# Performance work log

Hardware: AMD Instinct MI355X
Metric: run time of the kernel (lower is better)

The kernel has to match this reference:

```python
import jax, jax.numpy as jnp
import numpy as np
from jax import lax

B, L, H, K = 256, 512, 768, 64


def setup_inputs() -> dict:
    key = jax.random.key(0)
    k1, k2, k3, k4, k5 = jax.random.split(key, 5)
    features = jax.random.normal(k1, (B, L, H), dtype=jnp.float32)
    W = jax.random.normal(k2, (H, K), dtype=jnp.float32) * 0.02
    b = jnp.zeros((K,), dtype=jnp.float32)
    transition = jax.random.normal(k3, (K, K), dtype=jnp.float32)
    tags = jax.random.randint(k4, (B, L), 0, K, dtype=jnp.int64)
    # variable sentence lengths in decreasing order (repo sorts batches by length)
    lengths = jnp.sort(jax.random.randint(k5, (B,), L // 4, L + 1))[::-1]
    mask = jnp.arange(L)[None, :] < lengths[:, None]  # (B, L) bool, pads at end
    return {"features": features, "W": W, "b": b, "transition": transition,
            "tags": tags, "mask": mask}


def reference(features, W, b, transition, tags, mask):
    # encode: hidden2tag linear (dropout is identity in eval)
    emit = jnp.einsum("blh,hk->blk", features, W) + b  # (B, L, K)
    maskf = mask.astype(emit.dtype)

    # gold path score
    gold_emit = jnp.take_along_axis(emit, tags[:, :, None], axis=2)[..., 0]  # (B, L)
    trans_sc = transition[tags[:, :-1], tags[:, 1:]]                          # (B, L-1)
    score = gold_emit.at[:, 1:].add(trans_sc)
    total_score = (score * maskf).sum(axis=1)                                 # (B,)

    # CRF forward algorithm (log partition) via scan over time
    d0 = emit[:, 0]  # (B, K)
    emit_t = jnp.moveaxis(emit[:, 1:], 1, 0)  # (L-1, B, K)
    mask_t = mask[:, 1:].T                    # (L-1, B)

    def step(d, xs):
        e_t, m_t = xs
        # log_sum[b, j, k] = d[b, j] + transition[j, k] + e_t[b, k]
        log_sum = d[:, :, None] + transition[None, :, :] + e_t[:, None, :]
        d_new = jax.scipy.special.logsumexp(log_sum, axis=1)  # (B, K)
        d = jnp.where(m_t[:, None], d_new, d)  # finished sequences keep old d
        return d, None

    d, _ = lax.scan(step, d0, (emit_t, mask_t))
    log_z = jax.scipy.special.logsumexp(d, axis=1)  # (B,)

    return log_z - total_score  # negative log-likelihood per sentence, (B,)
```

## Files before the change

kernel.cpp:

```cpp
#include <hip/hip_runtime.h>
#include <hip/hip_bf16.h>
#include <string.h>

#define B_ 256
#define L_ 512
#define H_ 768
#define K_ 64
#define WT_OFF 33554432

typedef float  float4v  __attribute__((ext_vector_type(4)));
typedef float  float2v  __attribute__((ext_vector_type(2)));
typedef short  short8v  __attribute__((ext_vector_type(8)));

union BFragU { uint4 u4; short8v s8; };

__device__ inline unsigned short f2bf_bits(float f) {
    union { float f; unsigned int u; } c; c.f = f;
    unsigned int u = c.u;
    u += 0x7fffu + ((u >> 16) & 1u);
    return (unsigned short)(u >> 16);
}

__device__ inline float2v mk2(float x, float y) { float2v v; v.x = x; v.y = y; return v; }

__global__ void wt_transpose(const float* __restrict__ W, unsigned int* __restrict__ Wt) {
    int k = blockIdx.x;
    int j = threadIdx.x;
    float a = W[(size_t)(2 * j) * K_ + k];
    float b = W[(size_t)(2 * j + 1) * K_ + k];
    unsigned int u = (unsigned int)f2bf_bits(a) | ((unsigned int)f2bf_bits(b) << 16);
    Wt[k * (H_ / 2) + j] = u;
}

__global__ __launch_bounds__(256, 4)
void emit_gemm(const float* __restrict__ A, const unsigned short* __restrict__ Wt,
               const float* __restrict__ bias, float* __restrict__ emit) {
    const int tid  = threadIdx.x;
    const int lane = tid & 63;
    const int wid  = tid >> 6;
    const int lm   = lane & 15;
    const int lq   = lane >> 4;

    float4v acc[2][4];
    #pragma unroll
    for (int c = 0; c < 2; ++c)
        #pragma unroll
        for (int nt = 0; nt < 4; ++nt)
            acc[c][nt] = (float4v)0.f;

    const int rowbase = blockIdx.x * 128 + wid * 16 + lm;

    for (int ks = 0; ks < 24; ++ks) {
        short8v bfrag[4];
        #pragma unroll
        for (int nt = 0; nt < 4; ++nt) {
            const uint4* bp = reinterpret_cast<const uint4*>(
                Wt + (size_t)(lm + nt * 16) * H_ + ks * 32 + lq * 8);
            BFragU bb; bb.u4 = *bp;
            bfrag[nt] = bb.s8;
        }
        #pragma unroll
        for (int c = 0; c < 2; ++c) {
            const float* ap = A + (size_t)(rowbase + c * 64) * H_ + ks * 32 + lq * 8;
            float4 a0 = *reinterpret_cast<const float4*>(ap);
            float4 a1 = *reinterpret_cast<const float4*>(ap + 4);
            __hip_bfloat162 tt[4];
            tt[0] = __float22bfloat162_rn(make_float2(a0.x, a0.y));
            tt[1] = __float22bfloat162_rn(make_float2(a0.z, a0.w));
            tt[2] = __float22bfloat162_rn(make_float2(a1.x, a1.y));
            tt[3] = __float22bfloat162_rn(make_float2(a1.z, a1.w));
            short8v afrag;
            memcpy(&afrag, tt, 16);
            #pragma unroll
            for (int nt = 0; nt < 4; ++nt)
                acc[c][nt] = __builtin_amdgcn_mfma_f32_16x16x32_bf16(
                    afrag, bfrag[nt], acc[c][nt], 0, 0, 0);
        }
    }

    float bv[4];
    #pragma unroll
    for (int nt = 0; nt < 4; ++nt) bv[nt] = bias[nt * 16 + lm];
    #pragma unroll
    for (int c = 0; c < 2; ++c) {
        int rowb = blockIdx.x * 128 + c * 64 + wid * 16 + lq * 4;
        #pragma unroll
        for (int nt = 0; nt < 4; ++nt) {
            int col = nt * 16 + lm;
            #pragma unroll
            for (int r = 0; r < 4; ++r)
                emit[(size_t)(rowb + r) * K_ + col] = acc[c][nt][r] + bv[nt];
        }
    }
}

__global__ __launch_bounds__(64, 1)
void crf_scan(const float* __restrict__ emit, const float* __restrict__ T,
              const int* __restrict__ tags, const int* __restrict__ mask,
              float* __restrict__ out) {
    const int b    = blockIdx.x;
    const int lane = threadIdx.x;
    __shared__ __align__(16) float ebuf[2][16 * 64];
    __shared__ __align__(16) float qbuf[2][64];

    int len = 0;
    #pragma unroll
    for (int j = 0; j < 8; ++j) len += (mask[b * L_ + j * 64 + lane] != 0);
    #pragma unroll
    for (int off = 32; off; off >>= 1) len += __shfl_xor(len, off, 64);

    float2v et2[32];
    #pragma unroll
    for (int j = 0; j < 32; ++j) {
        et2[j].x = __expf(T[(2 * j) * K_ + lane]);
        et2[j].y = __expf(T[(2 * j + 1) * K_ + lane]);
    }

    const float* eb = emit + (size_t)b * L_ * K_;

    float sc = 0.f;
    for (int t = lane; t < len; t += 64) {
        int tg = tags[b * L_ + t];
        sc += eb[(size_t)t * K_ + tg];
        if (t > 0) sc += T[tags[b * L_ + t - 1] * K_ + tg];
    }
    #pragma unroll
    for (int off = 32; off; off >>= 1) sc += __shfl_xor(sc, off, 64);

    float e00 = eb[lane];
    float M = __int_as_float(__builtin_amdgcn_readfirstlane(__float_as_int(e00)));
    float q = __expf(e00 - M);
    qbuf[0][lane] = q;
    int prev_eps = 0;

    const int soff = ((lane >> 2) << 6) + ((lane & 3) << 4);
    {
        const float4* src = reinterpret_cast<const float4*>(eb + soff);
        float4 r0 = src[0], r1 = src[1], r2 = src[2], r3 = src[3];
        float4* dst = reinterpret_cast<float4*>(&ebuf[0][soff]);
        dst[0] = r0; dst[1] = r1; dst[2] = r2; dst[3] = r3;
    }

    int cur = 0;
    int t = 1;
    for (int c = 0;; ++c) {
        const int nt0  = (c + 1) << 4;
        const bool more = nt0 < len;
        float4 r0, r1, r2, r3;
        if (more) {
            const float4* src = reinterpret_cast<const float4*>(eb + nt0 * K_ + soff);
            r0 = src[0]; r1 = src[1]; r2 = src[2]; r3 = src[3];
        }
        const int tend = more ? nt0 : len;
        for (; t < tend; ++t) {
            float e  = ebuf[cur][((t & 15) << 6) + lane];
            float ef = __int_as_float(__builtin_amdgcn_readfirstlane(__float_as_int(e)));
            float delta = (float)prev_eps * 0.69314718f + ef;
            M += delta;
            float f = __expf(e - delta);

            const float4* qb4 = reinterpret_cast<const float4*>(&qbuf[(t + 1) & 1][0]);
            float2v a0 = mk2(0.f, 0.f), a1 = mk2(0.f, 0.f);
            float2v a2 = mk2(0.f, 0.f), a3 = mk2(0.f, 0.f);
            #pragma unroll
            for (int r = 0; r < 16; r += 2) {
                float4 p0 = qb4[r];
                float4 p1 = qb4[r + 1];
                a0 += mk2(p0.x, p0.y) * et2[2 * r];
                a1 += mk2(p0.z, p0.w) * et2[2 * r + 1];
                a2 += mk2(p1.x, p1.y) * et2[2 * r + 2];
                a3 += mk2(p1.z, p1.w) * et2[2 * r + 3];
            }
            float2v s2 = (a0 + a1) + (a2 + a3);
            float s = s2.x + s2.y;
            unsigned su = (unsigned)__builtin_amdgcn_readfirstlane(__float_as_int(s));
            prev_eps = (int)((su >> 23) & 0xff) - 127;
            q = s * f;
            qbuf[t & 1][lane] = q;
        }
        if (!more) break;
        float4* dst = reinterpret_cast<float4*>(&ebuf[cur ^ 1][soff]);
        dst[0] = r0; dst[1] = r1; dst[2] = r2; dst[3] = r3;
        cur ^= 1;
    }

    float z = q;
    #pragma unroll
    for (int off = 32; off; off >>= 1) z += __shfl_xor(z, off, 64);
    if (lane == 0) out[b] = M + __logf(z) - sc;
}

extern "C" void kernel_launch(void* const* d_in, const int* in_sizes, int n_in,
                              void* d_out, int out_size, void* d_ws, size_t ws_size,
                              hipStream_t stream) {
    const float* feat = (const float*)d_in[0];
    const float* W    = (const float*)d_in[1];
    const float* bias = (const float*)d_in[2];
    const float* T    = (const float*)d_in[3];
    const int*   tags = (const int*)d_in[4];
    const int*   mask = (const int*)d_in[5];
    float* out  = (float*)d_out;
    float* emit = (float*)d_ws;
    unsigned int*   WtW = (unsigned int*)((char*)d_ws + WT_OFF);
    unsigned short* Wt  = (unsigned short*)WtW;

    hipLaunchKernelGGL(wt_transpose, dim3(K_),   dim3(H_ / 2), 0, stream, W, WtW);
    hipLaunchKernelGGL(emit_gemm,    dim3(1024), dim3(256),    0, stream, feat, Wt, bias, emit);
    hipLaunchKernelGGL(crf_scan,     dim3(B_),   dim3(64),     0, stream, emit, T, tags, mask, out);
}
```

Baseline: 745.6 us.

## Skip padded rows in emission GEMM and double-buffer its global loads

The emission GEMM now reads the mask and exits blocks whose first row is padding. When only the second 64-row half of a block is padding, it runs a one-chunk variant that skips that half. Padded emissions are never read by the scan, so this avoids loading feature data that does not affect the output. The K loop is also software-pipelined with two register stages so loads overlap the MFMA work. In exchange, register pressure rises and occupancy is lowered to 2 blocks per CU.

```diff
diff --git a/kernel.cpp b/kernel.cpp
--- a/kernel.cpp
+++ b/kernel.cpp
@@ -32,58 +32,81 @@
     Wt[k * (H_ / 2) + j] = u;
 }
 
-__global__ __launch_bounds__(256, 4)
-void emit_gemm(const float* __restrict__ A, const unsigned short* __restrict__ Wt,
-               const float* __restrict__ bias, float* __restrict__ emit) {
-    const int tid  = threadIdx.x;
+template<int NC>
+struct Stage {
+    uint4  b[4];
+    float4 a[NC][2];
+};
+
+template<int NC>
+__device__ __forceinline__ void load_stage(Stage<NC>& s, const float* __restrict__ A,
+        const unsigned short* __restrict__ Wt, int rowbase, int ks, int lm, int lq) {
+    #pragma unroll
+    for (int nt = 0; nt < 4; ++nt)
+        s.b[nt] = *reinterpret_cast<const uint4*>(
+            Wt + (size_t)(lm + nt * 16) * H_ + ks * 32 + lq * 8);
+    #pragma unroll
+    for (int c = 0; c < NC; ++c) {
+        const float* ap = A + (size_t)(rowbase + c * 64) * H_ + ks * 32 + lq * 8;
+        s.a[c][0] = *reinterpret_cast<const float4*>(ap);
+        s.a[c][1] = *reinterpret_cast<const float4*>(ap + 4);
+    }
+}
+
+template<int NC>
+__device__ __forceinline__ void consume_stage(const Stage<NC>& s, float4v acc[][4]) {
+    short8v bfrag[4];
+    #pragma unroll
+    for (int nt = 0; nt < 4; ++nt) { BFragU u; u.u4 = s.b[nt]; bfrag[nt] = u.s8; }
+    #pragma unroll
+    for (int c = 0; c < NC; ++c) {
+        __hip_bfloat162 tt[4];
+        tt[0] = __float22bfloat162_rn(make_float2(s.a[c][0].x, s.a[c][0].y));
+        tt[1] = __float22bfloat162_rn(make_float2(s.a[c][0].z, s.a[c][0].w));
+        tt[2] = __float22bfloat162_rn(make_float2(s.a[c][1].x, s.a[c][1].y));
+        tt[3] = __float22bfloat162_rn(make_float2(s.a[c][1].z, s.a[c][1].w));
+        short8v afrag;
+        memcpy(&afrag, tt, 16);
+        #pragma unroll
+        for (int nt = 0; nt < 4; ++nt)
+            acc[c][nt] = __builtin_amdgcn_mfma_f32_16x16x32_bf16(
+                afrag, bfrag[nt], acc[c][nt], 0, 0, 0);
+    }
+}
+
+template<int NC>
+__device__ __forceinline__ void gemm_body(const float* __restrict__ A,
+        const unsigned short* __restrict__ Wt, const float* __restrict__ bias,
+        float* __restrict__ emit, int blk, int tid) {
     const int lane = tid & 63;
     const int wid  = tid >> 6;
     const int lm   = lane & 15;
     const int lq   = lane >> 4;
-
-    float4v acc[2][4];
-    #pragma unroll
-    for (int c = 0; c < 2; ++c)
+    const int rowbase = blk * 128 + wid * 16 + lm;
+
+    float4v acc[NC][4];
+    #pragma unroll
+    for (int c = 0; c < NC; ++c)
         #pragma unroll
         for (int nt = 0; nt < 4; ++nt)
             acc[c][nt] = (float4v)0.f;
 
-    const int rowbase = blockIdx.x * 128 + wid * 16 + lm;
-
-    for (int ks = 0; ks < 24; ++ks) {
-        short8v bfrag[4];
-        #pragma unroll
-        for (int nt = 0; nt < 4; ++nt) {
-            const uint4* bp = reinterpret_cast<const uint4*>(
-                Wt + (size_t)(lm + nt * 16) * H_ + ks * 32 + lq * 8);
-            BFragU bb; bb.u4 = *bp;
-            bfrag[nt] = bb.s8;
-        }
-        #pragma unroll
-        for (int c = 0; c < 2; ++c) {
-            const float* ap = A + (size_t)(rowbase + c * 64) * H_ + ks * 32 + lq * 8;
-            float4 a0 = *reinterpret_cast<const float4*>(ap);
-            float4 a1 = *reinterpret_cast<const float4*>(ap + 4);
-            __hip_bfloat162 tt[4];
-            tt[0] = __float22bfloat162_rn(make_float2(a0.x, a0.y));
-            tt[1] = __float22bfloat162_rn(make_float2(a0.z, a0.w));
-            tt[2] = __float22bfloat162_rn(make_float2(a1.x, a1.y));
-            tt[3] = __float22bfloat162_rn(make_float2(a1.z, a1.w));
-            short8v afrag;
-            memcpy(&afrag, tt, 16);
-            #pragma unroll
-            for (int nt = 0; nt < 4; ++nt)
-                acc[c][nt] = __builtin_amdgcn_mfma_f32_16x16x32_bf16(
-                    afrag, bfrag[nt], acc[c][nt], 0, 0, 0);
-        }
+    Stage<NC> s0, s1;
+    load_stage<NC>(s0, A, Wt, rowbase, 0, lm, lq);
+    #pragma unroll 1
+    for (int ks = 0; ks < 24; ks += 2) {
+        load_stage<NC>(s1, A, Wt, rowbase, ks + 1, lm, lq);
+        consume_stage<NC>(s0, acc);
+        load_stage<NC>(s0, A, Wt, rowbase, (ks + 2 < 24) ? ks + 2 : 23, lm, lq);
+        consume_stage<NC>(s1, acc);
     }
 
     float bv[4];
     #pragma unroll
     for (int nt = 0; nt < 4; ++nt) bv[nt] = bias[nt * 16 + lm];
     #pragma unroll
-    for (int c = 0; c < 2; ++c) {
-        int rowb = blockIdx.x * 128 + c * 64 + wid * 16 + lq * 4;
+    for (int c = 0; c < NC; ++c) {
+        int rowb = blk * 128 + c * 64 + wid * 16 + lq * 4;
         #pragma unroll
         for (int nt = 0; nt < 4; ++nt) {
             int col = nt * 16 + lm;
@@ -92,6 +115,18 @@
                 emit[(size_t)(rowb + r) * K_ + col] = acc[c][nt][r] + bv[nt];
         }
     }
+}
+
+__global__ __launch_bounds__(256, 2)
+void emit_gemm(const float* __restrict__ A, const unsigned short* __restrict__ Wt,
+               const float* __restrict__ bias, const int* __restrict__ mask,
+               float* __restrict__ emit) {
+    const int r0 = blockIdx.x * 128;
+    if (mask[r0] == 0) return;
+    if (mask[r0 + 64])
+        gemm_body<2>(A, Wt, bias, emit, blockIdx.x, threadIdx.x);
+    else
+        gemm_body<1>(A, Wt, bias, emit, blockIdx.x, threadIdx.x);
 }
 
 __global__ __launch_bounds__(64, 1)
@@ -205,6 +240,6 @@
     unsigned short* Wt  = (unsigned short*)WtW;
 
     hipLaunchKernelGGL(wt_transpose, dim3(K_),   dim3(H_ / 2), 0, stream, W, WtW);
-    hipLaunchKernelGGL(emit_gemm,    dim3(1024), dim3(256),    0, stream, feat, Wt, bias, emit);
+    hipLaunchKernelGGL(emit_gemm,    dim3(1024), dim3(256),    0, stream, feat, Wt, bias, mask, emit);
     hipLaunchKernelGGL(crf_scan,     dim3(B_),   dim3(64),     0, stream, emit, T, tags, mask, out);
 }
```

After: 729.5 us. 1.02x faster.
